# Performance work log

Measured on AMD Instinct MI355X. Metric: run time of the kernel, lower is better.

Reference implementation:

```python
import jax, jax.numpy as jnp
import numpy as np

D = 1024
H = 16
DH = D // H
BERT_EPS = 1e-12
LN_EPS = 1e-5


def _layernorm(x, gamma, beta, eps):
    mu = jnp.mean(x, axis=-1, keepdims=True)
    var = jnp.mean(jnp.square(x - mu), axis=-1, keepdims=True)
    return (x - mu) * jax.lax.rsqrt(var + eps) * gamma + beta


def setup_inputs() -> dict:
    key = jax.random.key(0)
    ks = jax.random.split(key, 12)
    s = 0.02
    return {
        "query_feat_2d": jax.random.normal(ks[0], (4096, D), jnp.float32),
        "video_feat_2d": jax.random.normal(ks[1], (1024, D), jnp.float32),
        "Wq": jax.random.normal(ks[2], (D, D), jnp.float32) * s,
        "bq": jnp.zeros((D,), jnp.float32),
        "Wk": jax.random.normal(ks[3], (D, D), jnp.float32) * s,
        "bk": jnp.zeros((D,), jnp.float32),
        "Wv": jax.random.normal(ks[4], (D, D), jnp.float32) * s,
        "bv": jnp.zeros((D,), jnp.float32),
        "Wo": jax.random.normal(ks[5], (D, D), jnp.float32) * s,
        "bo": jnp.zeros((D,), jnp.float32),
        "ln1_g": jnp.ones((D,), jnp.float32),
        "ln1_b": jnp.zeros((D,), jnp.float32),
        "ln2_g": jnp.ones((D,), jnp.float32),
        "ln2_b": jnp.zeros((D,), jnp.float32),
        "Wl": jax.random.normal(ks[6], (D, D), jnp.float32) * s,
        "bl": jnp.zeros((D,), jnp.float32),
    }


def reference(query_feat_2d, video_feat_2d, Wq, bq, Wk, bk, Wv, bv, Wo, bo,
              ln1_g, ln1_b, ln2_g, ln2_b, Wl, bl):
    Nq = query_feat_2d.shape[0]
    Nv = video_feat_2d.shape[0]
    # Projections; K/V computed ONCE (shared across all queries, avoiding the
    # redundant [N_q, N_v, D] expand the torch module materializes).
    Q = (query_feat_2d @ Wq + bq).reshape(Nq, H, DH)
    K = (video_feat_2d @ Wk + bk).reshape(Nv, H, DH)
    V = (video_feat_2d @ Wv + bv).reshape(Nv, H, DH)
    # Each query row is a length-1 sequence attending over all N_v video feats.
    scores = jnp.einsum("qhd,khd->hqk", Q, K) / jnp.sqrt(jnp.asarray(DH, Q.dtype))
    probs = jax.nn.softmax(scores, axis=-1)  # [H, Nq, Nv]
    ctx = jnp.einsum("hqk,khd->qhd", probs, V).reshape(Nq, D)
    # BertSelfOutput: dense + residual + LayerNorm
    att_out = ctx @ Wo + bo
    refined = _layernorm(att_out + query_feat_2d, ln1_g, ln1_b, BERT_EPS)
    # LinearLayer(layer_norm=True, relu=False): LN -> Linear
    final = _layernorm(refined, ln2_g, ln2_b, LN_EPS) @ Wl + bl
    return final
```

## Files before the change

kernel.cpp:

```cpp
#include <hip/hip_runtime.h>

static constexpr int D  = 1024;
static constexpr int NH = 16;
static constexpr int DH = 64;

using bf16x8 = __attribute__((ext_vector_type(8))) __bf16;
using bf16x4 = __attribute__((ext_vector_type(4))) __bf16;
using f32x4  = __attribute__((ext_vector_type(4))) float;

__global__ __launch_bounds__(256) void split_a(
    const float* __restrict__ X, __bf16* __restrict__ Xh, __bf16* __restrict__ Xl)
{
    const size_t i = ((size_t)blockIdx.x * 256 + threadIdx.x) * 8;
    float4 v0 = *(const float4*)&X[i];
    float4 v1 = *(const float4*)&X[i + 4];
    float f[8] = {v0.x, v0.y, v0.z, v0.w, v1.x, v1.y, v1.z, v1.w};
    bf16x8 h, l;
#pragma unroll
    for (int e = 0; e < 8; ++e) {
        __bf16 hi = (__bf16)f[e];
        h[e] = hi;
        l[e] = (__bf16)(f[e] - (float)hi);
    }
    *(bf16x8*)&Xh[i] = h;
    *(bf16x8*)&Xl[i] = l;
}

__global__ __launch_bounds__(256) void split_transpose_w(
    const float* __restrict__ W, float scale,
    __bf16* __restrict__ Th, __bf16* __restrict__ Tl)
{
    __shared__ float tile[32][33];
    const int t = threadIdx.x;
    const int r = t >> 3;
    const int c4 = (t & 7) << 2;
    const int n0 = blockIdx.x * 32, k0 = blockIdx.y * 32;

    float4 v = *(const float4*)&W[(size_t)(k0 + r) * 1024 + n0 + c4];
    tile[r][c4 + 0] = v.x; tile[r][c4 + 1] = v.y;
    tile[r][c4 + 2] = v.z; tile[r][c4 + 3] = v.w;
    __syncthreads();

    float f[4] = {tile[c4 + 0][r] * scale, tile[c4 + 1][r] * scale,
                  tile[c4 + 2][r] * scale, tile[c4 + 3][r] * scale};
    bf16x4 vh, vl;
#pragma unroll
    for (int e = 0; e < 4; ++e) {
        __bf16 hi = (__bf16)f[e];
        vh[e] = hi;
        vl[e] = (__bf16)(f[e] - (float)hi);
    }
    const size_t o = (size_t)(n0 + r) * 1024 + k0 + c4;
    *(bf16x4*)&Th[o] = vh;
    *(bf16x4*)&Tl[o] = vl;
}

template <bool SPLIT_OUT>
__global__ __launch_bounds__(256) void mfma_gemm_v3(
    const __bf16* __restrict__ Agh, const __bf16* __restrict__ Agl,
    const __bf16* __restrict__ BTh, const __bf16* __restrict__ BTl,
    const float* __restrict__ bias, float bscale,
    float* __restrict__ C, __bf16* __restrict__ Ch, __bf16* __restrict__ Cl)
{
    __shared__ alignas(16) __bf16 Ah[128][40], Al[128][40];
    __shared__ alignas(16) __bf16 Bh[128][40], Bl[128][40];

    const int tid = threadIdx.x;
    const int bm = blockIdx.y, bn = blockIdx.x;
    const int wave = tid >> 6, lane = tid & 63;
    const int wr = wave >> 1, wc = wave & 1;
    const int li = lane & 15, g = lane >> 4;

    const int ar = tid >> 1, ac = (tid & 1) << 4;

    f32x4 acc[4][4];
#pragma unroll
    for (int m = 0; m < 4; ++m)
#pragma unroll
        for (int n = 0; n < 4; ++n) acc[m][n] = (f32x4)0.f;

    for (int k0 = 0; k0 < 1024; k0 += 32) {
        __syncthreads();
        {
            const size_t oa = (size_t)(bm * 128 + ar) * 1024 + k0 + ac;
            *(bf16x8*)&Ah[ar][ac]     = *(const bf16x8*)(Agh + oa);
            *(bf16x8*)&Ah[ar][ac + 8] = *(const bf16x8*)(Agh + oa + 8);
            *(bf16x8*)&Al[ar][ac]     = *(const bf16x8*)(Agl + oa);
            *(bf16x8*)&Al[ar][ac + 8] = *(const bf16x8*)(Agl + oa + 8);
            const size_t ob = (size_t)(bn * 128 + ar) * 1024 + k0 + ac;
            *(bf16x8*)&Bh[ar][ac]     = *(const bf16x8*)(BTh + ob);
            *(bf16x8*)&Bh[ar][ac + 8] = *(const bf16x8*)(BTh + ob + 8);
            *(bf16x8*)&Bl[ar][ac]     = *(const bf16x8*)(BTl + ob);
            *(bf16x8*)&Bl[ar][ac + 8] = *(const bf16x8*)(BTl + ob + 8);
        }
        __syncthreads();

        bf16x8 fah[4], fal[4], fbh[4], fbl[4];
#pragma unroll
        for (int m = 0; m < 4; ++m) {
            fah[m] = *(const bf16x8*)&Ah[wr * 64 + m * 16 + li][g * 8];
            fal[m] = *(const bf16x8*)&Al[wr * 64 + m * 16 + li][g * 8];
        }
#pragma unroll
        for (int n = 0; n < 4; ++n) {
            fbh[n] = *(const bf16x8*)&Bh[wc * 64 + n * 16 + li][g * 8];
            fbl[n] = *(const bf16x8*)&Bl[wc * 64 + n * 16 + li][g * 8];
        }
#pragma unroll
        for (int m = 0; m < 4; ++m)
#pragma unroll
            for (int n = 0; n < 4; ++n) {
                acc[m][n] = __builtin_amdgcn_mfma_f32_16x16x32_bf16(fah[m], fbh[n], acc[m][n], 0, 0, 0);
                acc[m][n] = __builtin_amdgcn_mfma_f32_16x16x32_bf16(fah[m], fbl[n], acc[m][n], 0, 0, 0);
                acc[m][n] = __builtin_amdgcn_mfma_f32_16x16x32_bf16(fal[m], fbh[n], acc[m][n], 0, 0, 0);
            }
    }

#pragma unroll
    for (int m = 0; m < 4; ++m)
#pragma unroll
        for (int n = 0; n < 4; ++n) {
            const int col = bn * 128 + wc * 64 + n * 16 + li;
            const float bb = bias[col] * bscale;
#pragma unroll
            for (int e = 0; e < 4; ++e) {
                const int row = bm * 128 + wr * 64 + m * 16 + g * 4 + e;
                const float val = acc[m][n][e] + bb;
                if constexpr (SPLIT_OUT) {
                    __bf16 hi = (__bf16)val;
                    Ch[(size_t)row * 1024 + col] = hi;
                    Cl[(size_t)row * 1024 + col] = (__bf16)(val - (float)hi);
                } else {
                    C[(size_t)row * 1024 + col] = val;
                }
            }
        }
}

__global__ __launch_bounds__(256) void attn_mfma_kernel(
    const __bf16* __restrict__ Qhg, const __bf16* __restrict__ Qlg,
    const __bf16* __restrict__ Khg, const __bf16* __restrict__ Klg,
    const __bf16* __restrict__ Vhg, const __bf16* __restrict__ Vlg,
    __bf16* __restrict__ Ch, __bf16* __restrict__ Cl, int Nv)
{
    constexpr int PT = 72;
    __shared__ alignas(16) __bf16 KPh[64][PT], KPl[64][PT];
    __shared__ alignas(16) __bf16 Vth[64][PT], Vtl[64][PT];

    const int tid = threadIdx.x;
    const int h  = blockIdx.y;
    const int q0 = blockIdx.x * 64;
    const int wave = tid >> 6, lane = tid & 63;
    const int wr16 = wave * 16;
    const int li = lane & 15, g = lane >> 4;

    const int r = tid >> 2, c0 = (tid & 3) << 4;

    bf16x8 qah[2], qal[2];
    {
        const size_t qo = (size_t)(q0 + wr16 + li) * D + h * DH + g * 8;
        qah[0] = *(const bf16x8*)(Qhg + qo);
        qah[1] = *(const bf16x8*)(Qhg + qo + 32);
        qal[0] = *(const bf16x8*)(Qlg + qo);
        qal[1] = *(const bf16x8*)(Qlg + qo + 32);
    }

    float m_[4], l_[4];
    f32x4 o_acc[4];
#pragma unroll
    for (int e = 0; e < 4; ++e) { m_[e] = -1e30f; l_[e] = 0.f; }
#pragma unroll
    for (int n = 0; n < 4; ++n) o_acc[n] = (f32x4)0.f;

    for (int kt = 0; kt < Nv; kt += 64) {
        __syncthreads();
        {
            const size_t o = (size_t)(kt + r) * D + h * DH + c0;
            *(bf16x8*)&KPh[r][c0]     = *(const bf16x8*)(Khg + o);
            *(bf16x8*)&KPh[r][c0 + 8] = *(const bf16x8*)(Khg + o + 8);
            *(bf16x8*)&KPl[r][c0]     = *(const bf16x8*)(Klg + o);
            *(bf16x8*)&KPl[r][c0 + 8] = *(const bf16x8*)(Klg + o + 8);
            bf16x8 vh0 = *(const bf16x8*)(Vhg + o);
            bf16x8 vh1 = *(const bf16x8*)(Vhg + o + 8);
            bf16x8 vl0 = *(const bf16x8*)(Vlg + o);
            bf16x8 vl1 = *(const bf16x8*)(Vlg + o + 8);
#pragma unroll
            for (int e = 0; e < 8; ++e) {
                Vth[c0 + e][r]     = vh0[e];
                Vth[c0 + 8 + e][r] = vh1[e];
                Vtl[c0 + e][r]     = vl0[e];
                Vtl[c0 + 8 + e][r] = vl1[e];
            }
        }
        __syncthreads();

        f32x4 s_acc[4];
#pragma unroll
        for (int n = 0; n < 4; ++n) s_acc[n] = (f32x4)0.f;
#pragma unroll
        for (int n = 0; n < 4; ++n)
#pragma unroll
            for (int kk = 0; kk < 2; ++kk) {
                bf16x8 kh = *(const bf16x8*)&KPh[n * 16 + li][kk * 32 + g * 8];
                bf16x8 kl = *(const bf16x8*)&KPl[n * 16 + li][kk * 32 + g * 8];
                s_acc[n] = __builtin_amdgcn_mfma_f32_16x16x32_bf16(qah[kk], kh, s_acc[n], 0, 0, 0);
                s_acc[n] = __builtin_amdgcn_mfma_f32_16x16x32_bf16(qah[kk], kl, s_acc[n], 0, 0, 0);
                s_acc[n] = __builtin_amdgcn_mfma_f32_16x16x32_bf16(qal[kk], kh, s_acc[n], 0, 0, 0);
            }

        float rm[4];
#pragma unroll
        for (int e = 0; e < 4; ++e)
            rm[e] = fmaxf(fmaxf(s_acc[0][e], s_acc[1][e]),
                          fmaxf(s_acc[2][e], s_acc[3][e]));
#pragma unroll
        for (int off = 1; off < 16; off <<= 1)
#pragma unroll
            for (int e = 0; e < 4; ++e)
                rm[e] = fmaxf(rm[e], __shfl_xor(rm[e], off, 64));

        float resc[4], rs[4];
#pragma unroll
        for (int e = 0; e < 4; ++e) {
            float mn = fmaxf(m_[e], rm[e]);
            resc[e] = __expf(m_[e] - mn);
            m_[e] = mn;
        }
        float p[4][4];
#pragma unroll
        for (int n = 0; n < 4; ++n)
#pragma unroll
            for (int e = 0; e < 4; ++e)
                p[n][e] = __expf(s_acc[n][e] - m_[e]);
#pragma unroll
        for (int e = 0; e < 4; ++e)
            rs[e] = p[0][e] + p[1][e] + p[2][e] + p[3][e];
#pragma unroll
        for (int off = 1; off < 16; off <<= 1)
#pragma unroll
            for (int e = 0; e < 4; ++e)
                rs[e] += __shfl_xor(rs[e], off, 64);
#pragma unroll
        for (int e = 0; e < 4; ++e)
            l_[e] = l_[e] * resc[e] + rs[e];
#pragma unroll
        for (int n = 0; n < 4; ++n)
#pragma unroll
            for (int e = 0; e < 4; ++e)
                o_acc[n][e] *= resc[e];

        __syncthreads();

#pragma unroll
        for (int n = 0; n < 4; ++n)
#pragma unroll
            for (int e = 0; e < 4; ++e) {
                const int row = wr16 + g * 4 + e;
                const int col = n * 16 + li;
                float pv = p[n][e];
                __bf16 hi = (__bf16)pv;
                KPh[row][col] = hi;
                KPl[row][col] = (__bf16)(pv - (float)hi);
            }
        __syncthreads();

        bf16x8 pah[2], pal[2];
#pragma unroll
        for (int kk = 0; kk < 2; ++kk) {
            pah[kk] = *(const bf16x8*)&KPh[wr16 + li][kk * 32 + g * 8];
            pal[kk] = *(const bf16x8*)&KPl[wr16 + li][kk * 32 + g * 8];
        }
#pragma unroll
        for (int n = 0; n < 4; ++n)
#pragma unroll
            for (int kk = 0; kk < 2; ++kk) {
                bf16x8 vh = *(const bf16x8*)&Vth[n * 16 + li][kk * 32 + g * 8];
                bf16x8 vl = *(const bf16x8*)&Vtl[n * 16 + li][kk * 32 + g * 8];
                o_acc[n] = __builtin_amdgcn_mfma_f32_16x16x32_bf16(pah[kk], vh, o_acc[n], 0, 0, 0);
                o_acc[n] = __builtin_amdgcn_mfma_f32_16x16x32_bf16(pah[kk], vl, o_acc[n], 0, 0, 0);
                o_acc[n] = __builtin_amdgcn_mfma_f32_16x16x32_bf16(pal[kk], vh, o_acc[n], 0, 0, 0);
            }
    }

    float inv[4];
#pragma unroll
    for (int e = 0; e < 4; ++e) inv[e] = 1.f / l_[e];
#pragma unroll
    for (int n = 0; n < 4; ++n)
#pragma unroll
        for (int e = 0; e < 4; ++e) {
            const int row = q0 + wr16 + g * 4 + e;
            const int col = h * DH + n * 16 + li;
            const float val = o_acc[n][e] * inv[e];
            __bf16 hi = (__bf16)val;
            Ch[(size_t)row * D + col] = hi;
            Cl[(size_t)row * D + col] = (__bf16)(val - (float)hi);
        }
}

__global__ __launch_bounds__(256) void resid_dual_ln_kernel(
    const float* __restrict__ att, const float* __restrict__ resid,
    const float* __restrict__ g1, const float* __restrict__ b1,
    const float* __restrict__ g2, const float* __restrict__ b2,
    __bf16* __restrict__ Oh, __bf16* __restrict__ Ol)
{
    const int row = blockIdx.x;
    const int tid = threadIdx.x;
    const int c = tid << 2;
    const size_t base = (size_t)row * D + c;

    float4 a = *(const float4*)&att[base];
    float4 r = *(const float4*)&resid[base];
    float t[4] = {a.x + r.x, a.y + r.y, a.z + r.z, a.w + r.w};

    __shared__ float red[8];
    const int wid = tid >> 6, lane = tid & 63;

    float s = t[0] + t[1] + t[2] + t[3];
    float sq = t[0]*t[0] + t[1]*t[1] + t[2]*t[2] + t[3]*t[3];
#pragma unroll
    for (int off = 1; off < 64; off <<= 1) {
        s  += __shfl_xor(s, off, 64);
        sq += __shfl_xor(sq, off, 64);
    }
    if (lane == 0) { red[wid] = s; red[4 + wid] = sq; }
    __syncthreads();
    s  = red[0] + red[1] + red[2] + red[3];
    sq = red[4] + red[5] + red[6] + red[7];

    float mu  = s * (1.f / D);
    float var = sq * (1.f / D) - mu * mu;
    float rr  = rsqrtf(var + 1e-12f);

    float4 G1 = *(const float4*)&g1[c];
    float4 B1 = *(const float4*)&b1[c];
    float g1a[4] = {G1.x, G1.y, G1.z, G1.w};
    float b1a[4] = {B1.x, B1.y, B1.z, B1.w};
    float v[4];
#pragma unroll
    for (int j = 0; j < 4; ++j) v[j] = (t[j] - mu) * rr * g1a[j] + b1a[j];

    float s2 = v[0] + v[1] + v[2] + v[3];
    float q2 = v[0]*v[0] + v[1]*v[1] + v[2]*v[2] + v[3]*v[3];
#pragma unroll
    for (int off = 1; off < 64; off <<= 1) {
        s2 += __shfl_xor(s2, off, 64);
        q2 += __shfl_xor(q2, off, 64);
    }
    __syncthreads();
    if (lane == 0) { red[wid] = s2; red[4 + wid] = q2; }
    __syncthreads();
    s2 = red[0] + red[1] + red[2] + red[3];
    q2 = red[4] + red[5] + red[6] + red[7];

    float mu2  = s2 * (1.f / D);
    float var2 = q2 * (1.f / D) - mu2 * mu2;
    float r2   = rsqrtf(var2 + 1e-5f);

    float4 G2 = *(const float4*)&g2[c];
    float4 B2 = *(const float4*)&b2[c];
    float g2a[4] = {G2.x, G2.y, G2.z, G2.w};
    float b2a[4] = {B2.x, B2.y, B2.z, B2.w};
    bf16x4 oh, ol;
#pragma unroll
    for (int j = 0; j < 4; ++j) {
        float oo = (v[j] - mu2) * r2 * g2a[j] + b2a[j];
        __bf16 hi = (__bf16)oo;
        oh[j] = hi;
        ol[j] = (__bf16)(oo - (float)hi);
    }
    *(bf16x4*)&Oh[base] = oh;
    *(bf16x4*)&Ol[base] = ol;
}

extern "C" void kernel_launch(void* const* d_in, const int* in_sizes, int n_in,
                              void* d_out, int out_size, void* d_ws, size_t ws_size,
                              hipStream_t stream)
{
    const float* qf  = (const float*)d_in[0];
    const float* vf  = (const float*)d_in[1];
    const float* Wq  = (const float*)d_in[2];
    const float* bq  = (const float*)d_in[3];
    const float* Wk  = (const float*)d_in[4];
    const float* bk  = (const float*)d_in[5];
    const float* Wv  = (const float*)d_in[6];
    const float* bv  = (const float*)d_in[7];
    const float* Wo  = (const float*)d_in[8];
    const float* bo  = (const float*)d_in[9];
    const float* g1  = (const float*)d_in[10];
    const float* b1  = (const float*)d_in[11];
    const float* g2  = (const float*)d_in[12];
    const float* b2  = (const float*)d_in[13];
    const float* Wl  = (const float*)d_in[14];
    const float* bl  = (const float*)d_in[15];

    const int Nq = in_sizes[0] / D;
    const int Nv = in_sizes[1] / D;
    const size_t NQD = (size_t)Nq * D;
    const size_t NVD = (size_t)Nv * D;
    const size_t DD  = (size_t)D * D;

    char* base = (char*)d_ws;
    __bf16* R1h = (__bf16*)base;
    __bf16* R1l = R1h + NQD;
    __bf16* R2h = (__bf16*)(base + NQD * 4);
    __bf16* R2l = R2h + NQD;
    float*  att = (float*)R2h;
    __bf16* Ksh = (__bf16*)(base + NQD * 8);
    __bf16* Ksl = Ksh + NVD;
    __bf16* Vsh = Ksl + NVD;
    __bf16* Vsl = Vsh + NVD;
    __bf16* vfh = Vsl + NVD;
    __bf16* vfl = vfh + NVD;
    __bf16* Wth = vfl + NVD;
    __bf16* Wtl = Wth + DD;

    dim3 blk(256);
    const dim3 gW(32, 32);
    const dim3 gM(8, Nq / 128), gV(8, Nv / 128);

    split_a<<<dim3((unsigned)(NQD / 2048)), blk, 0, stream>>>(qf, R1h, R1l);
    split_a<<<dim3((unsigned)(NVD / 2048)), blk, 0, stream>>>(vf, vfh, vfl);

    split_transpose_w<<<gW, blk, 0, stream>>>(Wq, 0.125f, Wth, Wtl);
    mfma_gemm_v3<true><<<gM, blk, 0, stream>>>(R1h, R1l, Wth, Wtl, bq, 0.125f,
                                               nullptr, R2h, R2l);
    split_transpose_w<<<gW, blk, 0, stream>>>(Wk, 1.f, Wth, Wtl);
    mfma_gemm_v3<true><<<gV, blk, 0, stream>>>(vfh, vfl, Wth, Wtl, bk, 1.f,
                                               nullptr, Ksh, Ksl);
    split_transpose_w<<<gW, blk, 0, stream>>>(Wv, 1.f, Wth, Wtl);
    mfma_gemm_v3<true><<<gV, blk, 0, stream>>>(vfh, vfl, Wth, Wtl, bv, 1.f,
                                               nullptr, Vsh, Vsl);

    attn_mfma_kernel<<<dim3(Nq / 64, NH), blk, 0, stream>>>(
        R2h, R2l, Ksh, Ksl, Vsh, Vsl, R1h, R1l, Nv);

    split_transpose_w<<<gW, blk, 0, stream>>>(Wo, 1.f, Wth, Wtl);
    mfma_gemm_v3<false><<<gM, blk, 0, stream>>>(R1h, R1l, Wth, Wtl, bo, 1.f,
                                                att, nullptr, nullptr);

    resid_dual_ln_kernel<<<dim3(Nq), blk, 0, stream>>>(att, qf, g1, b1, g2, b2,
                                                       R1h, R1l);

    split_transpose_w<<<gW, blk, 0, stream>>>(Wl, 1.f, Wth, Wtl);
    mfma_gemm_v3<false><<<gM, blk, 0, stream>>>(R1h, R1l, Wth, Wtl, bl, 1.f,
                                                (float*)d_out, nullptr, nullptr);
}
```

Before: 479.8 us.

## Register-prefetch next K tile in GEMMs and attention; fuse K/V projections

```diff
diff --git a/kernel.cpp b/kernel.cpp
--- a/kernel.cpp
+++ b/kernel.cpp
@@ -56,7 +56,7 @@
 }
 
 template <bool SPLIT_OUT>
-__global__ __launch_bounds__(256) void mfma_gemm_v3(
+__global__ __launch_bounds__(256) void mfma_gemm_v4(
     const __bf16* __restrict__ Agh, const __bf16* __restrict__ Agl,
     const __bf16* __restrict__ BTh, const __bf16* __restrict__ BTl,
     const float* __restrict__ bias, float bscale,
@@ -79,21 +79,43 @@
 #pragma unroll
         for (int n = 0; n < 4; ++n) acc[m][n] = (f32x4)0.f;
 
+    const size_t oaBase = (size_t)(bm * 128 + ar) * 1024 + ac;
+    const size_t obBase = (size_t)(bn * 128 + ar) * 1024 + ac;
+
+    bf16x8 rah[2], ral[2], rbh[2], rbl[2];
+    rah[0] = *(const bf16x8*)(Agh + oaBase);
+    rah[1] = *(const bf16x8*)(Agh + oaBase + 8);
+    ral[0] = *(const bf16x8*)(Agl + oaBase);
+    ral[1] = *(const bf16x8*)(Agl + oaBase + 8);
+    rbh[0] = *(const bf16x8*)(BTh + obBase);
+    rbh[1] = *(const bf16x8*)(BTh + obBase + 8);
+    rbl[0] = *(const bf16x8*)(BTl + obBase);
+    rbl[1] = *(const bf16x8*)(BTl + obBase + 8);
+
     for (int k0 = 0; k0 < 1024; k0 += 32) {
         __syncthreads();
-        {
-            const size_t oa = (size_t)(bm * 128 + ar) * 1024 + k0 + ac;
-            *(bf16x8*)&Ah[ar][ac]     = *(const bf16x8*)(Agh + oa);
-            *(bf16x8*)&Ah[ar][ac + 8] = *(const bf16x8*)(Agh + oa + 8);
-            *(bf16x8*)&Al[ar][ac]     = *(const bf16x8*)(Agl + oa);
-            *(bf16x8*)&Al[ar][ac + 8] = *(const bf16x8*)(Agl + oa + 8);
-            const size_t ob = (size_t)(bn * 128 + ar) * 1024 + k0 + ac;
-            *(bf16x8*)&Bh[ar][ac]     = *(const bf16x8*)(BTh + ob);
-            *(bf16x8*)&Bh[ar][ac + 8] = *(const bf16x8*)(BTh + ob + 8);
-            *(bf16x8*)&Bl[ar][ac]     = *(const bf16x8*)(BTl + ob);
-            *(bf16x8*)&Bl[ar][ac + 8] = *(const bf16x8*)(BTl + ob + 8);
-        }
-        __syncthreads();
+        *(bf16x8*)&Ah[ar][ac]     = rah[0];
+        *(bf16x8*)&Ah[ar][ac + 8] = rah[1];
+        *(bf16x8*)&Al[ar][ac]     = ral[0];
+        *(bf16x8*)&Al[ar][ac + 8] = ral[1];
+        *(bf16x8*)&Bh[ar][ac]     = rbh[0];
+        *(bf16x8*)&Bh[ar][ac + 8] = rbh[1];
+        *(bf16x8*)&Bl[ar][ac]     = rbl[0];
+        *(bf16x8*)&Bl[ar][ac + 8] = rbl[1];
+        __syncthreads();
+
+        if (k0 + 32 < 1024) {
+            const size_t oa = oaBase + k0 + 32;
+            const size_t ob = obBase + k0 + 32;
+            rah[0] = *(const bf16x8*)(Agh + oa);
+            rah[1] = *(const bf16x8*)(Agh + oa + 8);
+            ral[0] = *(const bf16x8*)(Agl + oa);
+            ral[1] = *(const bf16x8*)(Agl + oa + 8);
+            rbh[0] = *(const bf16x8*)(BTh + ob);
+            rbh[1] = *(const bf16x8*)(BTh + ob + 8);
+            rbl[0] = *(const bf16x8*)(BTl + ob);
+            rbl[1] = *(const bf16x8*)(BTl + ob + 8);
+        }
 
         bf16x8 fah[4], fal[4], fbh[4], fbl[4];
 #pragma unroll
@@ -137,6 +159,113 @@
         }
 }
 
+__global__ __launch_bounds__(256) void mfma_gemm_kv(
+    const __bf16* __restrict__ Agh, const __bf16* __restrict__ Agl,
+    const __bf16* __restrict__ B1h, const __bf16* __restrict__ B1l,
+    const float* __restrict__ bias1, __bf16* __restrict__ C1h, __bf16* __restrict__ C1l,
+    const __bf16* __restrict__ B2h, const __bf16* __restrict__ B2l,
+    const float* __restrict__ bias2, __bf16* __restrict__ C2h, __bf16* __restrict__ C2l)
+{
+    const bool z = (blockIdx.z != 0);
+    const __bf16* BTh = z ? B2h : B1h;
+    const __bf16* BTl = z ? B2l : B1l;
+    const float*  bias = z ? bias2 : bias1;
+    __bf16* Ch = z ? C2h : C1h;
+    __bf16* Cl = z ? C2l : C1l;
+
+    __shared__ alignas(16) __bf16 Ah[128][40], Al[128][40];
+    __shared__ alignas(16) __bf16 Bh[128][40], Bl[128][40];
+
+    const int tid = threadIdx.x;
+    const int bm = blockIdx.y, bn = blockIdx.x;
+    const int wave = tid >> 6, lane = tid & 63;
+    const int wr = wave >> 1, wc = wave & 1;
+    const int li = lane & 15, g = lane >> 4;
+
+    const int ar = tid >> 1, ac = (tid & 1) << 4;
+
+    f32x4 acc[4][4];
+#pragma unroll
+    for (int m = 0; m < 4; ++m)
+#pragma unroll
+        for (int n = 0; n < 4; ++n) acc[m][n] = (f32x4)0.f;
+
+    const size_t oaBase = (size_t)(bm * 128 + ar) * 1024 + ac;
+    const size_t obBase = (size_t)(bn * 128 + ar) * 1024 + ac;
+
+    bf16x8 rah[2], ral[2], rbh[2], rbl[2];
+    rah[0] = *(const bf16x8*)(Agh + oaBase);
+    rah[1] = *(const bf16x8*)(Agh + oaBase + 8);
+    ral[0] = *(const bf16x8*)(Agl + oaBase);
+    ral[1] = *(const bf16x8*)(Agl + oaBase + 8);
+    rbh[0] = *(const bf16x8*)(BTh + obBase);
+    rbh[1] = *(const bf16x8*)(BTh + obBase + 8);
+    rbl[0] = *(const bf16x8*)(BTl + obBase);
+    rbl[1] = *(const bf16x8*)(BTl + obBase + 8);
+
+    for (int k0 = 0; k0 < 1024; k0 += 32) {
+        __syncthreads();
+        *(bf16x8*)&Ah[ar][ac]     = rah[0];
+        *(bf16x8*)&Ah[ar][ac + 8] = rah[1];
+        *(bf16x8*)&Al[ar][ac]     = ral[0];
+        *(bf16x8*)&Al[ar][ac + 8] = ral[1];
+        *(bf16x8*)&Bh[ar][ac]     = rbh[0];
+        *(bf16x8*)&Bh[ar][ac + 8] = rbh[1];
+        *(bf16x8*)&Bl[ar][ac]     = rbl[0];
+        *(bf16x8*)&Bl[ar][ac + 8] = rbl[1];
+        __syncthreads();
+
+        if (k0 + 32 < 1024) {
+            const size_t oa = oaBase + k0 + 32;
+            const size_t ob = obBase + k0 + 32;
+            rah[0] = *(const bf16x8*)(Agh + oa);
+            rah[1] = *(const bf16x8*)(Agh + oa + 8);
+            ral[0] = *(const bf16x8*)(Agl + oa);
+            ral[1] = *(const bf16x8*)(Agl + oa + 8);
+            rbh[0] = *(const bf16x8*)(BTh + ob);
+            rbh[1] = *(const bf16x8*)(BTh + ob + 8);
+            rbl[0] = *(const bf16x8*)(BTl + ob);
+            rbl[1] = *(const bf16x8*)(BTl + ob + 8);
+        }
+
+        bf16x8 fah[4], fal[4], fbh[4], fbl[4];
+#pragma unroll
+        for (int m = 0; m < 4; ++m) {
+            fah[m] = *(const bf16x8*)&Ah[wr * 64 + m * 16 + li][g * 8];
+            fal[m] = *(const bf16x8*)&Al[wr * 64 + m * 16 + li][g * 8];
+        }
+#pragma unroll
+        for (int n = 0; n < 4; ++n) {
+            fbh[n] = *(const bf16x8*)&Bh[wc * 64 + n * 16 + li][g * 8];
+            fbl[n] = *(const bf16x8*)&Bl[wc * 64 + n * 16 + li][g * 8];
+        }
+#pragma unroll
+        for (int m = 0; m < 4; ++m)
+#pragma unroll
+            for (int n = 0; n < 4; ++n) {
+                acc[m][n] = __builtin_amdgcn_mfma_f32_16x16x32_bf16(fah[m], fbh[n], acc[m][n], 0, 0, 0);
+                acc[m][n] = __builtin_amdgcn_mfma_f32_16x16x32_bf16(fah[m], fbl[n], acc[m][n], 0, 0, 0);
+                acc[m][n] = __builtin_amdgcn_mfma_f32_16x16x32_bf16(fal[m], fbh[n], acc[m][n], 0, 0, 0);
+            }
+    }
+
+#pragma unroll
+    for (int m = 0; m < 4; ++m)
+#pragma unroll
+        for (int n = 0; n < 4; ++n) {
+            const int col = bn * 128 + wc * 64 + n * 16 + li;
+            const float bb = bias[col];
+#pragma unroll
+            for (int e = 0; e < 4; ++e) {
+                const int row = bm * 128 + wr * 64 + m * 16 + g * 4 + e;
+                const float val = acc[m][n][e] + bb;
+                __bf16 hi = (__bf16)val;
+                Ch[(size_t)row * 1024 + col] = hi;
+                Cl[(size_t)row * 1024 + col] = (__bf16)(val - (float)hi);
+            }
+        }
+}
+
 __global__ __launch_bounds__(256) void attn_mfma_kernel(
     const __bf16* __restrict__ Qhg, const __bf16* __restrict__ Qlg,
     const __bf16* __restrict__ Khg, const __bf16* __restrict__ Klg,
@@ -155,6 +284,7 @@
     const int li = lane & 15, g = lane >> 4;
 
     const int r = tid >> 2, c0 = (tid & 3) << 4;
+    const size_t stBase = (size_t)r * D + h * DH + c0;
 
     bf16x8 qah[2], qal[2];
     {
@@ -165,6 +295,19 @@
         qal[1] = *(const bf16x8*)(Qlg + qo + 32);
     }
 
+    bf16x8 rkh[2], rkl[2], rvh[2], rvl[2];
+    {
+        const size_t o = stBase;
+        rkh[0] = *(const bf16x8*)(Khg + o);
+        rkh[1] = *(const bf16x8*)(Khg + o + 8);
+        rkl[0] = *(const bf16x8*)(Klg + o);
+        rkl[1] = *(const bf16x8*)(Klg + o + 8);
+        rvh[0] = *(const bf16x8*)(Vhg + o);
+        rvh[1] = *(const bf16x8*)(Vhg + o + 8);
+        rvl[0] = *(const bf16x8*)(Vlg + o);
+        rvl[1] = *(const bf16x8*)(Vlg + o + 8);
+    }
+
     float m_[4], l_[4];
     f32x4 o_acc[4];
 #pragma unroll
@@ -174,25 +317,30 @@
 
     for (int kt = 0; kt < Nv; kt += 64) {
         __syncthreads();
-        {
-            const size_t o = (size_t)(kt + r) * D + h * DH + c0;
-            *(bf16x8*)&KPh[r][c0]     = *(const bf16x8*)(Khg + o);
-            *(bf16x8*)&KPh[r][c0 + 8] = *(const bf16x8*)(Khg + o + 8);
-            *(bf16x8*)&KPl[r][c0]     = *(const bf16x8*)(Klg + o);
-            *(bf16x8*)&KPl[r][c0 + 8] = *(const bf16x8*)(Klg + o + 8);
-            bf16x8 vh0 = *(const bf16x8*)(Vhg + o);
-            bf16x8 vh1 = *(const bf16x8*)(Vhg + o + 8);
-            bf16x8 vl0 = *(const bf16x8*)(Vlg + o);
-            bf16x8 vl1 = *(const bf16x8*)(Vlg + o + 8);
-#pragma unroll
-            for (int e = 0; e < 8; ++e) {
-                Vth[c0 + e][r]     = vh0[e];
-                Vth[c0 + 8 + e][r] = vh1[e];
-                Vtl[c0 + e][r]     = vl0[e];
-                Vtl[c0 + 8 + e][r] = vl1[e];
-            }
-        }
-        __syncthreads();
+        *(bf16x8*)&KPh[r][c0]     = rkh[0];
+        *(bf16x8*)&KPh[r][c0 + 8] = rkh[1];
+        *(bf16x8*)&KPl[r][c0]     = rkl[0];
+        *(bf16x8*)&KPl[r][c0 + 8] = rkl[1];
+#pragma unroll
+        for (int e = 0; e < 8; ++e) {
+            Vth[c0 + e][r]     = rvh[0][e];
+            Vth[c0 + 8 + e][r] = rvh[1][e];
+            Vtl[c0 + e][r]     = rvl[0][e];
+            Vtl[c0 + 8 + e][r] = rvl[1][e];
+        }
+        __syncthreads();
+
+        if (kt + 64 < Nv) {
+            const size_t o = stBase + (size_t)(kt + 64) * D;
+            rkh[0] = *(const bf16x8*)(Khg + o);
+            rkh[1] = *(const bf16x8*)(Khg + o + 8);
+            rkl[0] = *(const bf16x8*)(Klg + o);
+            rkl[1] = *(const bf16x8*)(Klg + o + 8);
+            rvh[0] = *(const bf16x8*)(Vhg + o);
+            rvh[1] = *(const bf16x8*)(Vhg + o + 8);
+            rvl[0] = *(const bf16x8*)(Vlg + o);
+            rvl[1] = *(const bf16x8*)(Vlg + o + 8);
+        }
 
         f32x4 s_acc[4];
 #pragma unroll
@@ -412,37 +560,42 @@
     __bf16* Vsl = Vsh + NVD;
     __bf16* vfh = Vsl + NVD;
     __bf16* vfl = vfh + NVD;
-    __bf16* Wth = vfl + NVD;
-    __bf16* Wtl = Wth + DD;
+    __bf16* W1h = vfl + NVD;
+    __bf16* W1l = W1h + DD;
+    __bf16* W2h = W1l + DD;
+    __bf16* W2l = W2h + DD;
+    __bf16* W3h = W2l + DD;
+    __bf16* W3l = W3h + DD;
 
     dim3 blk(256);
     const dim3 gW(32, 32);
-    const dim3 gM(8, Nq / 128), gV(8, Nv / 128);
+    const dim3 gM(8, Nq / 128);
+    const dim3 gKV(8, Nv / 128, 2);
 
     split_a<<<dim3((unsigned)(NQD / 2048)), blk, 0, stream>>>(qf, R1h, R1l);
     split_a<<<dim3((unsigned)(NVD / 2048)), blk, 0, stream>>>(vf, vfh, vfl);
 
-    split_transpose_w<<<gW, blk, 0, stream>>>(Wq, 0.125f, Wth, Wtl);
-    mfma_gemm_v3<true><<<gM, blk, 0, stream>>>(R1h, R1l, Wth, Wtl, bq, 0.125f,
+    split_transpose_w<<<gW, blk, 0, stream>>>(Wq, 0.125f, W1h, W1l);
+    split_transpose_w<<<gW, blk, 0, stream>>>(Wk, 1.f,    W2h, W2l);
+    split_transpose_w<<<gW, blk, 0, stream>>>(Wv, 1.f,    W3h, W3l);
+
+    mfma_gemm_v4<true><<<gM, blk, 0, stream>>>(R1h, R1l, W1h, W1l, bq, 0.125f,
                                                nullptr, R2h, R2l);
-    split_transpose_w<<<gW, blk, 0, stream>>>(Wk, 1.f, Wth, Wtl);
-    mfma_gemm_v3<true><<<gV, blk, 0, stream>>>(vfh, vfl, Wth, Wtl, bk, 1.f,
-                                               nullptr, Ksh, Ksl);
-    split_transpose_w<<<gW, blk, 0, stream>>>(Wv, 1.f, Wth, Wtl);
-    mfma_gemm_v3<true><<<gV, blk, 0, stream>>>(vfh, vfl, Wth, Wtl, bv, 1.f,
-                                               nullptr, Vsh, Vsl);
+    mfma_gemm_kv<<<gKV, blk, 0, stream>>>(vfh, vfl,
+                                          W2h, W2l, bk, Ksh, Ksl,
+                                          W3h, W3l, bv, Vsh, Vsl);
 
     attn_mfma_kernel<<<dim3(Nq / 64, NH), blk, 0, stream>>>(
         R2h, R2l, Ksh, Ksl, Vsh, Vsl, R1h, R1l, Nv);
 
-    split_transpose_w<<<gW, blk, 0, stream>>>(Wo, 1.f, Wth, Wtl);
-    mfma_gemm_v3<false><<<gM, blk, 0, stream>>>(R1h, R1l, Wth, Wtl, bo, 1.f,
+    split_transpose_w<<<gW, blk, 0, stream>>>(Wo, 1.f, W1h, W1l);
+    mfma_gemm_v4<false><<<gM, blk, 0, stream>>>(R1h, R1l, W1h, W1l, bo, 1.f,
                                                 att, nullptr, nullptr);
 
     resid_dual_ln_kernel<<<dim3(Nq), blk, 0, stream>>>(att, qf, g1, b1, g2, b2,
                                                        R1h, R1l);
 
-    split_transpose_w<<<gW, blk, 0, stream>>>(Wl, 1.f, Wth, Wtl);
-    mfma_gemm_v3<false><<<gM, blk, 0, stream>>>(R1h, R1l, Wth, Wtl, bl, 1.f,
+    split_transpose_w<<<gW, blk, 0, stream>>>(Wl, 1.f, W1h, W1l);
+    mfma_gemm_v4<false><<<gM, blk, 0, stream>>>(R1h, R1l, W1h, W1l, bl, 1.f,
                                                 (float*)d_out, nullptr, nullptr);
 }
```

After: 412.6 us. 1.16x faster.
